# Performance work log

Hardware: AMD Instinct MI355X
Metric: run time of the kernel (lower is better)

Reference implementation:

```python
import jax, jax.numpy as jnp
import numpy as np

N = 32768      # nodes
E = 262144     # edges
G = 256        # graphs
D_IN, D_H, D_OUT = 256, 512, 512
STEPS = 3      # set2set processing steps


def setup_inputs() -> dict:
    key = jax.random.key(0)
    ks = jax.random.split(key, 10)
    x = jax.random.normal(ks[0], (N, D_IN), jnp.float32)
    edge_index = jax.random.randint(ks[1], (2, E), 0, N, dtype=jnp.int64)
    batch = jnp.sort(jax.random.randint(ks[2], (N,), 0, G, dtype=jnp.int64))
    W1 = jax.random.normal(ks[3], (D_IN, D_H), jnp.float32) * (1.0 / np.sqrt(D_IN))
    b1 = jnp.zeros((D_H,), jnp.float32)
    W2 = jax.random.normal(ks[4], (D_H, D_OUT), jnp.float32) * (1.0 / np.sqrt(D_H))
    b2 = jnp.zeros((D_OUT,), jnp.float32)
    # LSTM(input=2*D_OUT, hidden=D_OUT); gate order i,f,g,o (PyTorch)
    s = 1.0 / np.sqrt(D_OUT)
    W_ih = jax.random.uniform(ks[5], (4 * D_OUT, 2 * D_OUT), jnp.float32, -s, s)
    W_hh = jax.random.uniform(ks[6], (4 * D_OUT, D_OUT), jnp.float32, -s, s)
    b_ih = jax.random.uniform(ks[7], (4 * D_OUT,), jnp.float32, -s, s)
    b_hh = jax.random.uniform(ks[8], (4 * D_OUT,), jnp.float32, -s, s)
    return {"x": x, "edge_index": edge_index, "batch": batch,
            "W1": W1, "b1": b1, "W2": W2, "b2": b2,
            "W_ih": W_ih, "W_hh": W_hh, "b_ih": b_ih, "b_hh": b_hh}


def _gcn_conv(x, src, dst, norm, W, b):
    # GCNConv: symmetric-normalized aggregation of linearly transformed features
    h = x @ W                              # [N, d_out]
    msg = h[src] * norm[:, None]           # gather + scale  [E+N, d_out]
    agg = jax.ops.segment_sum(msg, dst, num_segments=N)
    return agg + b


def reference(x, edge_index, batch, W1, b1, W2, b2, W_ih, W_hh, b_ih, b_hh):
    # --- GCN normalization with self-loops: D^-1/2 (A+I) D^-1/2 ---
    loop = jnp.arange(N, dtype=edge_index.dtype)
    src = jnp.concatenate([edge_index[0], loop])
    dst = jnp.concatenate([edge_index[1], loop])
    deg = jax.ops.segment_sum(jnp.ones_like(src, x.dtype), dst, num_segments=N)
    dinv = jax.lax.rsqrt(deg)              # deg >= 1 thanks to self-loops
    norm = dinv[src] * dinv[dst]

    h = jax.nn.relu(_gcn_conv(x, src, dst, norm, W1, b1))
    h = _gcn_conv(h, src, dst, norm, W2, b2)   # [N, D_OUT]

    # --- Set2Set pooling (3 processing steps) ---
    d = D_OUT
    q_star = jnp.zeros((G, 2 * d), h.dtype)
    hs = jnp.zeros((G, d), h.dtype)
    cs = jnp.zeros((G, d), h.dtype)
    for _ in range(STEPS):
        gates = q_star @ W_ih.T + b_ih + hs @ W_hh.T + b_hh
        i, f, g, o = jnp.split(gates, 4, axis=-1)
        cs = jax.nn.sigmoid(f) * cs + jax.nn.sigmoid(i) * jnp.tanh(g)
        hs = jax.nn.sigmoid(o) * jnp.tanh(cs)      # query q  [G, d]
        e = jnp.sum(h * hs[batch], axis=-1)        # [N]
        emax = jax.ops.segment_max(e, batch, num_segments=G)
        emax = jnp.where(jnp.isfinite(emax), emax, 0.0)
        ex = jnp.exp(e - emax[batch])
        denom = jax.ops.segment_sum(ex, batch, num_segments=G)
        a = ex / jnp.maximum(denom, 1e-12)[batch]  # per-graph softmax
        r = jax.ops.segment_sum(a[:, None] * h, batch, num_segments=G)
        q_star = jnp.concatenate([hs, r], axis=-1)  # [G, 2d]
    return q_star
```

## Files before the change

kernel.cpp:

```cpp
#include <hip/hip_runtime.h>
#include <math.h>

#define NN 32768
#define NE 262144
#define NG 256
#define DIN 256
#define DH 512
#define DOUT 512

typedef unsigned short u16;
typedef _Float16 f16;
typedef __attribute__((ext_vector_type(4))) _Float16 f16x4;
typedef __attribute__((ext_vector_type(8))) _Float16 f16x8;
typedef __attribute__((ext_vector_type(4))) float f32x4;

__device__ inline void split2h(float f, f16& h, f16& l) {
  h = (f16)f;
  l = (f16)(f - (float)h);
}

__device__ inline void gload16(const void* g, void* l) {
  __builtin_amdgcn_global_load_lds((const __attribute__((address_space(1))) unsigned int*)g,
                                   (__attribute__((address_space(3))) unsigned int*)l,
                                   16, 0, 0);
}


__global__ void k_count(const int* __restrict__ ei, int* __restrict__ counts) {
  int e = blockIdx.x * 256 + threadIdx.x;
  if (e < NE) atomicAdd(&counts[ei[NE + e]], 1);
}

__global__ __launch_bounds__(128) void k_scanA(const int* __restrict__ counts,
                                               int* __restrict__ bsum) {
  int b = blockIdx.x, t = threadIdx.x;
  int v = counts[b * 128 + t];
  __shared__ int red[128];
  red[t] = v;
  __syncthreads();
#pragma unroll
  for (int o = 64; o > 0; o >>= 1) {
    if (t < o) red[t] += red[t + o];
    __syncthreads();
  }
  if (t == 0) bsum[b] = red[0];
}

__global__ __launch_bounds__(256) void k_scanB(const int* __restrict__ bsum,
                                               int* __restrict__ boff,
                                               int* __restrict__ offs) {
  __shared__ int s[256];
  int t = threadIdx.x;
  int v = bsum[t];
  s[t] = v;
  __syncthreads();
  for (int o = 1; o < 256; o <<= 1) {
    int add = (t >= o) ? s[t - o] : 0;
    __syncthreads();
    s[t] += add;
    __syncthreads();
  }
  boff[t] = s[t] - v;
  if (t == 255) offs[NN] = s[255];
}

__global__ __launch_bounds__(128) void k_scanC(const int* __restrict__ counts,
                                               const int* __restrict__ boff,
                                               int* __restrict__ offs,
                                               float* __restrict__ dinv) {
  int b = blockIdx.x, t = threadIdx.x;
  int v = counts[b * 128 + t];
  __shared__ int s[128];
  s[t] = v;
  __syncthreads();
  for (int o = 1; o < 128; o <<= 1) {
    int add = (t >= o) ? s[t - o] : 0;
    __syncthreads();
    s[t] += add;
    __syncthreads();
  }
  offs[b * 128 + t] = boff[b] + s[t] - v;
  dinv[b * 128 + t] = rsqrtf((float)(v + 1));
}

__global__ void k_fill(const int* __restrict__ ei, const int* __restrict__ offs,
                       int* __restrict__ cursor, int* __restrict__ csr) {
  int e = blockIdx.x * 256 + threadIdx.x;
  if (e < NE) {
    int d = ei[NE + e];
    int pos = offs[d] + atomicAdd(&cursor[d], 1);
    csr[pos] = ei[e];
  }
}

__global__ void k_prep(const float* __restrict__ x, f16* __restrict__ xh,
                       const float* __restrict__ W1, f16* __restrict__ w1th,
                       const float* __restrict__ W2, f16* __restrict__ w2th,
                       const float* __restrict__ W_ih, const float* __restrict__ W_hh,
                       f16* __restrict__ wgh,
                       const int* __restrict__ batch, int* __restrict__ starts) {
  int b = blockIdx.x;
  if (b < 8192) {
    int i = (b * 256 + threadIdx.x) << 2;
    float4 v = *(const float4*)(x + i);
    f16x4 h = {(f16)v.x, (f16)v.y, (f16)v.z, (f16)v.w};
    *(f16x4*)(xh + i) = h;
  } else if (b < 8704) {
    int idx = (b - 8192) * 256 + threadIdx.x;
    int k = idx >> 9, n = idx & 511;
    w1th[(size_t)n * DIN + k] = (f16)W1[idx];
  } else if (b < 9728) {
    int idx = (b - 8704) * 256 + threadIdx.x;
    int k = idx >> 9, n = idx & 511;
    w2th[(size_t)n * DH + k] = (f16)W2[idx];
  } else if (b < 17920) {
    int idx = (b - 9728) * 256 + threadIdx.x;
    int n = idx >> 10, c = idx & 1023;
    float v = W_ih[(size_t)n * 1024 + c];
    if (c < 512) v += W_hh[(size_t)n * 512 + c];
    wgh[idx] = (f16)v;
  } else {
    int g = threadIdx.x;
    int lo = 0, hi = NN;
    while (lo < hi) {
      int mid = (lo + hi) >> 1;
      if (batch[mid] < g) lo = mid + 1; else hi = mid;
    }
    starts[g] = lo;
    if (g == 0) starts[NG] = NN;
  }
}

template <int MODE>
__global__ __launch_bounds__(256) void k_mfma_gemm(
    const f16* __restrict__ Ahi, const f16* __restrict__ Alo,
    const f16* __restrict__ Bhi,
    float* __restrict__ C, f16* __restrict__ Chi, f16* __restrict__ Clo,
    f16* __restrict__ Cf16, const float* __restrict__ bias,
    int M, int N, int K, int lda, int ldb) {
  __shared__ char lds[49152];

  int nbn = N >> 7;
  int nwg = (M >> 7) * nbn;
  int b = blockIdx.x;
  int slice = b / nwg;
  b -= slice * nwg;
  int koff = slice * K;
  int swz = (b & 7) * (nwg >> 3) + (b >> 3);
  int bn = (swz % nbn) << 7;
  int bm = (swz / nbn) << 7;

  int tid = threadIdx.x;
  int w = tid >> 6, lane = tid & 63;
  int wm = (w >> 1) << 6, wn = (w & 1) << 6;
  int fr = lane & 15;
  int fq = lane >> 4;

  f32x4 acc[4][4];
#pragma unroll
  for (int i = 0; i < 4; ++i)
#pragma unroll
    for (int j = 0; j < 4; ++j) acc[i][j] = (f32x4){0.f, 0.f, 0.f, 0.f};

  for (int ks = 0; ks < K; ks += 64) {
#pragma unroll
    for (int i = 0; i < 4; ++i) {
      int L = i * 256 + tid;
      int row = L >> 3;
      int ke = ((L & 7) ^ (row & 7)) << 3;
      int ldsoff = i * 4096 + w * 1024;
      gload16(Ahi + (size_t)(bm + row) * lda + koff + ks + ke, lds + ldsoff);
      gload16(Alo + (size_t)(bm + row) * lda + koff + ks + ke, lds + 16384 + ldsoff);
      gload16(Bhi + (size_t)(bn + row) * ldb + koff + ks + ke, lds + 32768 + ldsoff);
    }
    __syncthreads();
#pragma unroll
    for (int kk = 0; kk < 2; ++kk) {
      f16x8 ah[4], al[4], bh[4];
#pragma unroll
      for (int m = 0; m < 4; ++m) {
        int row = wm + m * 16 + fr;
        int boff = row * 128 + (((kk << 6) + (fq << 4)) ^ ((row & 7) << 4));
        ah[m] = *(const f16x8*)(lds + boff);
        al[m] = *(const f16x8*)(lds + 16384 + boff);
      }
#pragma unroll
      for (int n = 0; n < 4; ++n) {
        int row = wn + n * 16 + fr;
        int boff = row * 128 + (((kk << 6) + (fq << 4)) ^ ((row & 7) << 4));
        bh[n] = *(const f16x8*)(lds + 32768 + boff);
      }
#pragma unroll
      for (int m = 0; m < 4; ++m)
#pragma unroll
        for (int n = 0; n < 4; ++n) {
          acc[m][n] = __builtin_amdgcn_mfma_f32_16x16x32_f16(ah[m], bh[n], acc[m][n], 0, 0, 0);
          acc[m][n] = __builtin_amdgcn_mfma_f32_16x16x32_f16(al[m], bh[n], acc[m][n], 0, 0, 0);
        }
    }
    __syncthreads();
  }
#pragma unroll
  for (int m = 0; m < 4; ++m)
#pragma unroll
    for (int n = 0; n < 4; ++n)
#pragma unroll
      for (int i = 0; i < 4; ++i) {
        int r = bm + wm + m * 16 + fq * 4 + i;
        int c = bn + wn + n * 16 + fr;
        float val = acc[m][n][i];
        if (MODE == 1) {
          val += bias[c];
          val = fmaxf(val, 0.f);
          f16 h, l;
          split2h(val, h, l);
          Chi[(size_t)r * N + c] = h;
          Clo[(size_t)r * N + c] = l;
        } else if (MODE == 2) {
          Cf16[(size_t)r * N + c] = (f16)val;
        } else {
          C[(size_t)slice * M * N + (size_t)r * N + c] = val;
        }
      }
}

__global__ __launch_bounds__(256) void k_agg256(const f16* __restrict__ xh,
                                                const int* __restrict__ offs,
                                                const int* __restrict__ csr,
                                                const float* __restrict__ dinv,
                                                f16* __restrict__ ohi, f16* __restrict__ olo) {
  int wv = threadIdx.x >> 6, lane = threadIdx.x & 63;
  int v = blockIdx.x * 4 + wv;
  int f = lane << 2;
  int s = offs[v], t = offs[v + 1];
  float dv = dinv[v];
  f16x4 rs = *(const f16x4*)(xh + (size_t)v * DIN + f);
  float a0[4] = {}, a1[4] = {}, a2[4] = {}, a3[4] = {};
  for (int base = s; base < t; base += 64) {
    int rem = min(64, t - base);
    int idx = (lane < rem) ? csr[base + lane] : 0;
    float wl = (lane < rem) ? dinv[idx] : 0.f;
    int i = 0;
    for (; i + 7 < rem; i += 8) {
      int u[8]; float ww[8]; f16x4 r[8];
#pragma unroll
      for (int q = 0; q < 8; ++q) { u[q] = __shfl(idx, i + q); ww[q] = __shfl(wl, i + q); }
#pragma unroll
      for (int q = 0; q < 8; ++q) r[q] = *(const f16x4*)(xh + (size_t)u[q] * DIN + f);
#pragma unroll
      for (int k = 0; k < 4; ++k) {
        a0[k] += ww[0] * (float)r[0][k]; a1[k] += ww[1] * (float)r[1][k];
        a2[k] += ww[2] * (float)r[2][k]; a3[k] += ww[3] * (float)r[3][k];
        a0[k] += ww[4] * (float)r[4][k]; a1[k] += ww[5] * (float)r[5][k];
        a2[k] += ww[6] * (float)r[6][k]; a3[k] += ww[7] * (float)r[7][k];
      }
    }
    for (; i + 1 < rem; i += 2) {
      int u0 = __shfl(idx, i), u1 = __shfl(idx, i + 1);
      float w0 = __shfl(wl, i), w1 = __shfl(wl, i + 1);
      f16x4 r0 = *(const f16x4*)(xh + (size_t)u0 * DIN + f);
      f16x4 r1 = *(const f16x4*)(xh + (size_t)u1 * DIN + f);
#pragma unroll
      for (int k = 0; k < 4; ++k) { a0[k] += w0 * (float)r0[k]; a1[k] += w1 * (float)r1[k]; }
    }
    if (i < rem) {
      int u0 = __shfl(idx, i);
      float w0 = __shfl(wl, i);
      f16x4 r0 = *(const f16x4*)(xh + (size_t)u0 * DIN + f);
#pragma unroll
      for (int k = 0; k < 4; ++k) a0[k] += w0 * (float)r0[k];
    }
  }
  f16x4 vh, vl;
#pragma unroll
  for (int k = 0; k < 4; ++k) {
    float r = (a0[k] + a1[k] + a2[k] + a3[k] + dv * (float)rs[k]) * dv;
    f16 h, l;
    split2h(r, h, l);
    vh[k] = h; vl[k] = l;
  }
  *(f16x4*)(ohi + (size_t)v * DIN + f) = vh;
  *(f16x4*)(olo + (size_t)v * DIN + f) = vl;
}

__global__ __launch_bounds__(256) void k_agg512(const f16* __restrict__ T2,
                                                const int* __restrict__ offs,
                                                const int* __restrict__ csr,
                                                const float* __restrict__ dinv,
                                                const float* __restrict__ bias,
                                                f16* __restrict__ H2) {
  int wv = threadIdx.x >> 6, lane = threadIdx.x & 63;
  int v = blockIdx.x * 4 + wv;
  int f = lane << 3;
  int s = offs[v], t = offs[v + 1];
  float dv = dinv[v];
  f16x8 rs = *(const f16x8*)(T2 + (size_t)v * DH + f);
  float a0[8] = {}, a1[8] = {}, a2[8] = {}, a3[8] = {};
  for (int base = s; base < t; base += 64) {
    int rem = min(64, t - base);
    int idx = (lane < rem) ? csr[base + lane] : 0;
    float wl = (lane < rem) ? dinv[idx] : 0.f;
    int i = 0;
    for (; i + 7 < rem; i += 8) {
      int u[8]; float ww[8]; f16x8 r[8];
#pragma unroll
      for (int q = 0; q < 8; ++q) { u[q] = __shfl(idx, i + q); ww[q] = __shfl(wl, i + q); }
#pragma unroll
      for (int q = 0; q < 8; ++q) r[q] = *(const f16x8*)(T2 + (size_t)u[q] * DH + f);
#pragma unroll
      for (int k = 0; k < 8; ++k) {
        a0[k] += ww[0] * (float)r[0][k]; a1[k] += ww[1] * (float)r[1][k];
        a2[k] += ww[2] * (float)r[2][k]; a3[k] += ww[3] * (float)r[3][k];
        a0[k] += ww[4] * (float)r[4][k]; a1[k] += ww[5] * (float)r[5][k];
        a2[k] += ww[6] * (float)r[6][k]; a3[k] += ww[7] * (float)r[7][k];
      }
    }
    for (; i + 1 < rem; i += 2) {
      int u0 = __shfl(idx, i), u1 = __shfl(idx, i + 1);
      float w0 = __shfl(wl, i), w1 = __shfl(wl, i + 1);
      f16x8 r0 = *(const f16x8*)(T2 + (size_t)u0 * DH + f);
      f16x8 r1 = *(const f16x8*)(T2 + (size_t)u1 * DH + f);
#pragma unroll
      for (int k = 0; k < 8; ++k) { a0[k] += w0 * (float)r0[k]; a1[k] += w1 * (float)r1[k]; }
    }
    if (i < rem) {
      int u0 = __shfl(idx, i);
      float w0 = __shfl(wl, i);
      f16x8 r0 = *(const f16x8*)(T2 + (size_t)u0 * DH + f);
#pragma unroll
      for (int k = 0; k < 8; ++k) a0[k] += w0 * (float)r0[k];
    }
  }
  float4 bb0 = *(const float4*)(bias + f);
  float4 bb1 = *(const float4*)(bias + f + 4);
  float bbv[8] = {bb0.x, bb0.y, bb0.z, bb0.w, bb1.x, bb1.y, bb1.z, bb1.w};
  f16x8 out;
#pragma unroll
  for (int k = 0; k < 8; ++k)
    out[k] = (f16)((a0[k] + a1[k] + a2[k] + a3[k] + dv * (float)rs[k]) * dv + bbv[k]);
  *(f16x8*)(H2 + (size_t)v * DH + f) = out;
}

__global__ __launch_bounds__(512) void k_step(const float* __restrict__ gp,
                                              const float* __restrict__ b_ih,
                                              const float* __restrict__ b_hh,
                                              float* __restrict__ cs,
                                              const f16* __restrict__ H2,
                                              const int* __restrict__ starts,
                                              float* __restrict__ qstar,
                                              f16* __restrict__ qhhi, f16* __restrict__ qhlo) {
  int g = blockIdx.x;
  int tid = threadIdx.x, wv = tid >> 6, lane = tid & 63;
  __shared__ float shs[512];
  __shared__ float lm[8], lsum[8];
  __shared__ float lr[8][512];

  {
    int j = tid;
    const float* g0 = gp + (size_t)g * 2048;
    float iv = b_ih[j]        + b_hh[j];
    float fv = b_ih[512 + j]  + b_hh[512 + j];
    float gv = b_ih[1024 + j] + b_hh[1024 + j];
    float ov = b_ih[1536 + j] + b_hh[1536 + j];
#pragma unroll
    for (int sl = 0; sl < 4; ++sl) {
      const float* gs = g0 + (size_t)sl * 524288;
      iv += gs[j]; fv += gs[512 + j]; gv += gs[1024 + j]; ov += gs[1536 + j];
    }
    float si = 1.f / (1.f + expf(-iv));
    float sf = 1.f / (1.f + expf(-fv));
    float so = 1.f / (1.f + expf(-ov));
    float c = sf * cs[(size_t)g * 512 + j] + si * tanhf(gv);
    float h = so * tanhf(c);
    cs[(size_t)g * 512 + j] = c;
    shs[j] = h;
    qstar[(size_t)g * 1024 + j] = h;
    f16 hh, hl;
    split2h(h, hh, hl);
    qhhi[(size_t)g * 1024 + j] = hh;
    qhlo[(size_t)g * 1024 + j] = hl;
  }
  __syncthreads();

  int s = starts[g], t = starts[g + 1];
  int cnt = t - s;
  float hsr[8];
#pragma unroll
  for (int k = 0; k < 8; ++k) hsr[k] = shs[lane * 8 + k];

  float m = -INFINITY, ssum = 0.f;
  float racc[8] = {};
  f16x8 rv = {};
  if (wv < cnt) rv = *(const f16x8*)(H2 + (size_t)(s + wv) * DH + lane * 8);
  for (int i = wv; i < cnt; i += 8) {
    f16x8 cur = rv;
    if (i + 8 < cnt) rv = *(const f16x8*)(H2 + (size_t)(s + i + 8) * DH + lane * 8);
    float e = 0.f;
#pragma unroll
    for (int k = 0; k < 8; ++k) e += (float)cur[k] * hsr[k];
#pragma unroll
    for (int o = 1; o < 64; o <<= 1) e += __shfl_xor(e, o);
    float mn = fmaxf(m, e);
    float scale = expf(m - mn);
    float p = expf(e - mn);
    ssum = ssum * scale + p;
#pragma unroll
    for (int k = 0; k < 8; ++k) racc[k] = racc[k] * scale + p * (float)cur[k];
    m = mn;
  }
  if (lane == 0) { lm[wv] = m; lsum[wv] = ssum; }
#pragma unroll
  for (int k = 0; k < 8; ++k) lr[wv][lane * 8 + k] = racc[k];
  __syncthreads();
  float M = -INFINITY;
#pragma unroll
  for (int w2 = 0; w2 < 8; ++w2) M = fmaxf(M, lm[w2]);
  if (!(M > -3.0e38f)) M = 0.f;
  float denom = 0.f;
  float sc[8];
#pragma unroll
  for (int w2 = 0; w2 < 8; ++w2) { sc[w2] = expf(lm[w2] - M); denom += lsum[w2] * sc[w2]; }
  float inv = 1.f / fmaxf(denom, 1e-12f);
  int f = tid;
  float r = 0.f;
#pragma unroll
  for (int w2 = 0; w2 < 8; ++w2) r += lr[w2][f] * sc[w2];
  r *= inv;
  qstar[(size_t)g * 1024 + 512 + f] = r;
  f16 h0, l0;
  split2h(r, h0, l0);
  qhhi[(size_t)g * 1024 + 512 + f] = h0;
  qhlo[(size_t)g * 1024 + 512 + f] = l0;
}

extern "C" void kernel_launch(void* const* d_in, const int* in_sizes, int n_in,
                              void* d_out, int out_size, void* d_ws, size_t ws_size,
                              hipStream_t stream) {
  const float* x     = (const float*)d_in[0];
  const int*   ei    = (const int*)d_in[1];
  const int*   batch = (const int*)d_in[2];
  const float* W1    = (const float*)d_in[3];
  const float* b1    = (const float*)d_in[4];
  const float* W2    = (const float*)d_in[5];
  const float* b2    = (const float*)d_in[6];
  const float* W_ih  = (const float*)d_in[7];
  const float* W_hh  = (const float*)d_in[8];
  const float* b_ih  = (const float*)d_in[9];
  const float* b_hh  = (const float*)d_in[10];
  float* qstar = (float*)d_out;

  char* w = (char*)d_ws;
  size_t off = 0;
  auto carve = [&](size_t bytes) -> void* {
    void* p = w + off;
    off += (bytes + 255) & ~(size_t)255;
    return p;
  };
  f16* xh      = (f16*)carve((size_t)NN * DIN * 2);
  f16* axhi    = (f16*)carve((size_t)NN * DIN * 2);
  f16* axlo    = (f16*)carve((size_t)NN * DIN * 2);
  f16* h1hi    = (f16*)carve((size_t)NN * DH * 2);
  f16* h1lo    = (f16*)carve((size_t)NN * DH * 2);
  f16* t2h     = (f16*)carve((size_t)NN * DH * 2);
  f16* H2h     = (f16*)carve((size_t)NN * DH * 2);
  f16* w1th    = (f16*)carve((size_t)DH * DIN * 2);
  f16* w2th    = (f16*)carve((size_t)DH * DH * 2);
  f16* wgh     = (f16*)carve((size_t)2048 * 1024 * 2);
  float* gp    = (float*)carve((size_t)4 * NG * 2048 * 4);
  int* counts  = (int*)carve((size_t)NN * 4);
  int* cursor  = (int*)carve((size_t)NN * 4);
  float* cs    = (float*)carve((size_t)NG * DOUT * 4);
  f16* qhhi    = (f16*)carve((size_t)NG * 1024 * 2);
  f16* qhlo    = (f16*)carve((size_t)NG * 1024 * 2);
  int* offs    = (int*)carve((size_t)(NN + 1) * 4);
  int* csr     = (int*)carve((size_t)NE * 4);
  float* dinv  = (float*)carve((size_t)NN * 4);
  int* starts  = (int*)carve((size_t)(NG + 1) * 4);
  int* bsum    = (int*)carve((size_t)256 * 4);
  int* boff    = (int*)carve((size_t)256 * 4);

  hipMemsetAsync(counts, 0, (size_t)2 * NN * 4, stream);
  hipMemsetAsync(cs, 0, (size_t)NG * DOUT * 4 + (size_t)2 * NG * 1024 * 2, stream);

  k_prep<<<17921, 256, 0, stream>>>(x, xh, W1, w1th, W2, w2th, W_ih, W_hh, wgh, batch, starts);
  k_count<<<NE / 256, 256, 0, stream>>>(ei, counts);
  k_scanA<<<NN / 128, 128, 0, stream>>>(counts, bsum);
  k_scanB<<<1, 256, 0, stream>>>(bsum, boff, offs);
  k_scanC<<<NN / 128, 128, 0, stream>>>(counts, boff, offs, dinv);
  k_fill<<<NE / 256, 256, 0, stream>>>(ei, offs, cursor, csr);

  k_agg256<<<NN / 4, 256, 0, stream>>>(xh, offs, csr, dinv, axhi, axlo);
  k_mfma_gemm<1><<<(NN / 128) * (DH / 128), 256, 0, stream>>>(
      axhi, axlo, w1th, nullptr, h1hi, h1lo, nullptr, b1, NN, DH, DIN, DIN, DIN);
  k_mfma_gemm<2><<<(NN / 128) * (DH / 128), 256, 0, stream>>>(
      h1hi, h1lo, w2th, nullptr, nullptr, nullptr, t2h, nullptr, NN, DH, DH, DH, DH);
  k_agg512<<<NN / 4, 256, 0, stream>>>(t2h, offs, csr, dinv, b2, H2h);

  for (int step = 0; step < 3; ++step) {
    k_mfma_gemm<0><<<4 * (NG / 128) * (2048 / 128), 256, 0, stream>>>(
        qhhi, qhlo, wgh, gp, nullptr, nullptr, nullptr, nullptr,
        NG, 2048, 256, 1024, 1024);
    k_step<<<NG, 512, 0, stream>>>(gp, b_ih, b_hh, cs, H2h, starts, qstar, qhhi, qhlo);
  }
}
```

Measured before the change: 263.5 us.

## Drop hi/lo split for GCN GEMMs, split agg512 by columns, deepen gate split-K

Removes the two-term fp16 hi/lo error compensation from the aggregated-feature and hidden-layer GEMMs, so they read one fp16 operand, issue half the MFMAs and write single fp16 outputs. The 512-wide aggregation is split into two launches of 256 columns each, giving each lane smaller loads and fewer registers. The set2set gate GEMM moves from 4 to 8 split-K slices for more parallelism, and the LSTM step sums 8 partials. The cost is lower precision in the GCN layers and extra partial-sum traffic in the gate path.

```diff
diff --git a/kernel.cpp b/kernel.cpp
--- a/kernel.cpp
+++ b/kernel.cpp
@@ -131,14 +131,14 @@
   }
 }
 
-template <int MODE>
+template <int MODE, int TERMS>
 __global__ __launch_bounds__(256) void k_mfma_gemm(
     const f16* __restrict__ Ahi, const f16* __restrict__ Alo,
     const f16* __restrict__ Bhi,
-    float* __restrict__ C, f16* __restrict__ Chi, f16* __restrict__ Clo,
-    f16* __restrict__ Cf16, const float* __restrict__ bias,
+    float* __restrict__ C, f16* __restrict__ Cf16, const float* __restrict__ bias,
     int M, int N, int K, int lda, int ldb) {
-  __shared__ char lds[49152];
+  constexpr int BOFF = (TERMS == 2) ? 32768 : 16384;
+  __shared__ char lds[(TERMS == 2) ? 49152 : 32768];
 
   int nbn = N >> 7;
   int nwg = (M >> 7) * nbn;
@@ -170,8 +170,9 @@
       int ke = ((L & 7) ^ (row & 7)) << 3;
       int ldsoff = i * 4096 + w * 1024;
       gload16(Ahi + (size_t)(bm + row) * lda + koff + ks + ke, lds + ldsoff);
-      gload16(Alo + (size_t)(bm + row) * lda + koff + ks + ke, lds + 16384 + ldsoff);
-      gload16(Bhi + (size_t)(bn + row) * ldb + koff + ks + ke, lds + 32768 + ldsoff);
+      if (TERMS == 2)
+        gload16(Alo + (size_t)(bm + row) * lda + koff + ks + ke, lds + 16384 + ldsoff);
+      gload16(Bhi + (size_t)(bn + row) * ldb + koff + ks + ke, lds + BOFF + ldsoff);
     }
     __syncthreads();
 #pragma unroll
@@ -182,20 +183,21 @@
         int row = wm + m * 16 + fr;
         int boff = row * 128 + (((kk << 6) + (fq << 4)) ^ ((row & 7) << 4));
         ah[m] = *(const f16x8*)(lds + boff);
-        al[m] = *(const f16x8*)(lds + 16384 + boff);
+        if (TERMS == 2) al[m] = *(const f16x8*)(lds + 16384 + boff);
       }
 #pragma unroll
       for (int n = 0; n < 4; ++n) {
         int row = wn + n * 16 + fr;
         int boff = row * 128 + (((kk << 6) + (fq << 4)) ^ ((row & 7) << 4));
-        bh[n] = *(const f16x8*)(lds + 32768 + boff);
+        bh[n] = *(const f16x8*)(lds + BOFF + boff);
       }
 #pragma unroll
       for (int m = 0; m < 4; ++m)
 #pragma unroll
         for (int n = 0; n < 4; ++n) {
           acc[m][n] = __builtin_amdgcn_mfma_f32_16x16x32_f16(ah[m], bh[n], acc[m][n], 0, 0, 0);
-          acc[m][n] = __builtin_amdgcn_mfma_f32_16x16x32_f16(al[m], bh[n], acc[m][n], 0, 0, 0);
+          if (TERMS == 2)
+            acc[m][n] = __builtin_amdgcn_mfma_f32_16x16x32_f16(al[m], bh[n], acc[m][n], 0, 0, 0);
         }
     }
     __syncthreads();
@@ -212,10 +214,7 @@
         if (MODE == 1) {
           val += bias[c];
           val = fmaxf(val, 0.f);
-          f16 h, l;
-          split2h(val, h, l);
-          Chi[(size_t)r * N + c] = h;
-          Clo[(size_t)r * N + c] = l;
+          Cf16[(size_t)r * N + c] = (f16)val;
         } else if (MODE == 2) {
           Cf16[(size_t)r * N + c] = (f16)val;
         } else {
@@ -228,7 +227,7 @@
                                                 const int* __restrict__ offs,
                                                 const int* __restrict__ csr,
                                                 const float* __restrict__ dinv,
-                                                f16* __restrict__ ohi, f16* __restrict__ olo) {
+                                                f16* __restrict__ oh) {
   int wv = threadIdx.x >> 6, lane = threadIdx.x & 63;
   int v = blockIdx.x * 4 + wv;
   int f = lane << 2;
@@ -271,16 +270,11 @@
       for (int k = 0; k < 4; ++k) a0[k] += w0 * (float)r0[k];
     }
   }
-  f16x4 vh, vl;
-#pragma unroll
-  for (int k = 0; k < 4; ++k) {
-    float r = (a0[k] + a1[k] + a2[k] + a3[k] + dv * (float)rs[k]) * dv;
-    f16 h, l;
-    split2h(r, h, l);
-    vh[k] = h; vl[k] = l;
-  }
-  *(f16x4*)(ohi + (size_t)v * DIN + f) = vh;
-  *(f16x4*)(olo + (size_t)v * DIN + f) = vl;
+  f16x4 vh;
+#pragma unroll
+  for (int k = 0; k < 4; ++k)
+    vh[k] = (f16)((a0[k] + a1[k] + a2[k] + a3[k] + dv * (float)rs[k]) * dv);
+  *(f16x4*)(oh + (size_t)v * DIN + f) = vh;
 }
 
 __global__ __launch_bounds__(256) void k_agg512(const f16* __restrict__ T2,
@@ -288,27 +282,27 @@
                                                 const int* __restrict__ csr,
                                                 const float* __restrict__ dinv,
                                                 const float* __restrict__ bias,
-                                                f16* __restrict__ H2) {
+                                                f16* __restrict__ H2, int colbase) {
   int wv = threadIdx.x >> 6, lane = threadIdx.x & 63;
   int v = blockIdx.x * 4 + wv;
-  int f = lane << 3;
+  int f = colbase + (lane << 2);
   int s = offs[v], t = offs[v + 1];
   float dv = dinv[v];
-  f16x8 rs = *(const f16x8*)(T2 + (size_t)v * DH + f);
-  float a0[8] = {}, a1[8] = {}, a2[8] = {}, a3[8] = {};
+  f16x4 rs = *(const f16x4*)(T2 + (size_t)v * DH + f);
+  float a0[4] = {}, a1[4] = {}, a2[4] = {}, a3[4] = {};
   for (int base = s; base < t; base += 64) {
     int rem = min(64, t - base);
     int idx = (lane < rem) ? csr[base + lane] : 0;
     float wl = (lane < rem) ? dinv[idx] : 0.f;
     int i = 0;
     for (; i + 7 < rem; i += 8) {
-      int u[8]; float ww[8]; f16x8 r[8];
+      int u[8]; float ww[8]; f16x4 r[8];
 #pragma unroll
       for (int q = 0; q < 8; ++q) { u[q] = __shfl(idx, i + q); ww[q] = __shfl(wl, i + q); }
 #pragma unroll
-      for (int q = 0; q < 8; ++q) r[q] = *(const f16x8*)(T2 + (size_t)u[q] * DH + f);
-#pragma unroll
-      for (int k = 0; k < 8; ++k) {
+      for (int q = 0; q < 8; ++q) r[q] = *(const f16x4*)(T2 + (size_t)u[q] * DH + f);
+#pragma unroll
+      for (int k = 0; k < 4; ++k) {
         a0[k] += ww[0] * (float)r[0][k]; a1[k] += ww[1] * (float)r[1][k];
         a2[k] += ww[2] * (float)r[2][k]; a3[k] += ww[3] * (float)r[3][k];
         a0[k] += ww[4] * (float)r[4][k]; a1[k] += ww[5] * (float)r[5][k];
@@ -318,27 +312,26 @@
     for (; i + 1 < rem; i += 2) {
       int u0 = __shfl(idx, i), u1 = __shfl(idx, i + 1);
       float w0 = __shfl(wl, i), w1 = __shfl(wl, i + 1);
-      f16x8 r0 = *(const f16x8*)(T2 + (size_t)u0 * DH + f);
-      f16x8 r1 = *(const f16x8*)(T2 + (size_t)u1 * DH + f);
-#pragma unroll
-      for (int k = 0; k < 8; ++k) { a0[k] += w0 * (float)r0[k]; a1[k] += w1 * (float)r1[k]; }
+      f16x4 r0 = *(const f16x4*)(T2 + (size_t)u0 * DH + f);
+      f16x4 r1 = *(const f16x4*)(T2 + (size_t)u1 * DH + f);
+#pragma unroll
+      for (int k = 0; k < 4; ++k) { a0[k] += w0 * (float)r0[k]; a1[k] += w1 * (float)r1[k]; }
     }
     if (i < rem) {
       int u0 = __shfl(idx, i);
       float w0 = __shfl(wl, i);
-      f16x8 r0 = *(const f16x8*)(T2 + (size_t)u0 * DH + f);
-#pragma unroll
-      for (int k = 0; k < 8; ++k) a0[k] += w0 * (float)r0[k];
-    }
-  }
-  float4 bb0 = *(const float4*)(bias + f);
-  float4 bb1 = *(const float4*)(bias + f + 4);
-  float bbv[8] = {bb0.x, bb0.y, bb0.z, bb0.w, bb1.x, bb1.y, bb1.z, bb1.w};
-  f16x8 out;
-#pragma unroll
-  for (int k = 0; k < 8; ++k)
+      f16x4 r0 = *(const f16x4*)(T2 + (size_t)u0 * DH + f);
+#pragma unroll
+      for (int k = 0; k < 4; ++k) a0[k] += w0 * (float)r0[k];
+    }
+  }
+  float4 bb = *(const float4*)(bias + f);
+  float bbv[4] = {bb.x, bb.y, bb.z, bb.w};
+  f16x4 out;
+#pragma unroll
+  for (int k = 0; k < 4; ++k)
     out[k] = (f16)((a0[k] + a1[k] + a2[k] + a3[k] + dv * (float)rs[k]) * dv + bbv[k]);
-  *(f16x8*)(H2 + (size_t)v * DH + f) = out;
+  *(f16x4*)(H2 + (size_t)v * DH + f) = out;
 }
 
 __global__ __launch_bounds__(512) void k_step(const float* __restrict__ gp,
@@ -363,7 +356,7 @@
     float gv = b_ih[1024 + j] + b_hh[1024 + j];
     float ov = b_ih[1536 + j] + b_hh[1536 + j];
 #pragma unroll
-    for (int sl = 0; sl < 4; ++sl) {
+    for (int sl = 0; sl < 8; ++sl) {
       const float* gs = g0 + (size_t)sl * 524288;
       iv += gs[j]; fv += gs[512 + j]; gv += gs[1024 + j]; ov += gs[1536 + j];
     }
@@ -457,16 +450,14 @@
     return p;
   };
   f16* xh      = (f16*)carve((size_t)NN * DIN * 2);
-  f16* axhi    = (f16*)carve((size_t)NN * DIN * 2);
-  f16* axlo    = (f16*)carve((size_t)NN * DIN * 2);
-  f16* h1hi    = (f16*)carve((size_t)NN * DH * 2);
-  f16* h1lo    = (f16*)carve((size_t)NN * DH * 2);
+  f16* axh     = (f16*)carve((size_t)NN * DIN * 2);
+  f16* h1h     = (f16*)carve((size_t)NN * DH * 2);
   f16* t2h     = (f16*)carve((size_t)NN * DH * 2);
   f16* H2h     = (f16*)carve((size_t)NN * DH * 2);
   f16* w1th    = (f16*)carve((size_t)DH * DIN * 2);
   f16* w2th    = (f16*)carve((size_t)DH * DH * 2);
   f16* wgh     = (f16*)carve((size_t)2048 * 1024 * 2);
-  float* gp    = (float*)carve((size_t)4 * NG * 2048 * 4);
+  float* gp    = (float*)carve((size_t)8 * NG * 2048 * 4);
   int* counts  = (int*)carve((size_t)NN * 4);
   int* cursor  = (int*)carve((size_t)NN * 4);
   float* cs    = (float*)carve((size_t)NG * DOUT * 4);
@@ -489,17 +480,17 @@
   k_scanC<<<NN / 128, 128, 0, stream>>>(counts, boff, offs, dinv);
   k_fill<<<NE / 256, 256, 0, stream>>>(ei, offs, cursor, csr);
 
-  k_agg256<<<NN / 4, 256, 0, stream>>>(xh, offs, csr, dinv, axhi, axlo);
-  k_mfma_gemm<1><<<(NN / 128) * (DH / 128), 256, 0, stream>>>(
-      axhi, axlo, w1th, nullptr, h1hi, h1lo, nullptr, b1, NN, DH, DIN, DIN, DIN);
-  k_mfma_gemm<2><<<(NN / 128) * (DH / 128), 256, 0, stream>>>(
-      h1hi, h1lo, w2th, nullptr, nullptr, nullptr, t2h, nullptr, NN, DH, DH, DH, DH);
-  k_agg512<<<NN / 4, 256, 0, stream>>>(t2h, offs, csr, dinv, b2, H2h);
+  k_agg256<<<NN / 4, 256, 0, stream>>>(xh, offs, csr, dinv, axh);
+  k_mfma_gemm<1, 1><<<(NN / 128) * (DH / 128), 256, 0, stream>>>(
+      axh, nullptr, w1th, nullptr, h1h, b1, NN, DH, DIN, DIN, DIN);
+  k_mfma_gemm<2, 1><<<(NN / 128) * (DH / 128), 256, 0, stream>>>(
+      h1h, nullptr, w2th, nullptr, t2h, nullptr, NN, DH, DH, DH, DH);
+  k_agg512<<<NN / 4, 256, 0, stream>>>(t2h, offs, csr, dinv, b2, H2h, 0);
+  k_agg512<<<NN / 4, 256, 0, stream>>>(t2h, offs, csr, dinv, b2, H2h, 256);
 
   for (int step = 0; step < 3; ++step) {
-    k_mfma_gemm<0><<<4 * (NG / 128) * (2048 / 128), 256, 0, stream>>>(
-        qhhi, qhlo, wgh, gp, nullptr, nullptr, nullptr, nullptr,
-        NG, 2048, 256, 1024, 1024);
+    k_mfma_gemm<0, 2><<<8 * (NG / 128) * (2048 / 128), 256, 0, stream>>>(
+        qhhi, qhlo, wgh, gp, nullptr, nullptr, NG, 2048, 128, 1024, 1024);
     k_step<<<NG, 512, 0, stream>>>(gp, b_ih, b_hh, cs, H2h, starts, qstar, qhhi, qhlo);
   }
 }
```

New measurement: 247.7 us. 1.06x faster.
